# Optimization experiments

Measured on AMD Instinct MI355X. Metric: run time of the kernel, lower is better.

The kernel has to match this reference:

```python
import jax, jax.numpy as jnp
import numpy as np

N, M, D, K = 32768, 8192, 384, 9


def setup_inputs() -> dict:
    key = jax.random.key(0)
    k1, k2 = jax.random.split(key)
    return {
        "embedding": jax.random.normal(k1, (N, D), dtype=jnp.float32),
        "memory_bank": jax.random.normal(k2, (M, D), dtype=jnp.float32),
        "n_neighbors": K,
    }


def reference(embedding, memory_bank, n_neighbors):
    x_norm = jnp.sum(embedding * embedding, axis=-1, keepdims=True)      # [N, 1]
    y_norm = jnp.sum(memory_bank * memory_bank, axis=-1, keepdims=True)  # [M, 1]
    d2 = x_norm - 2.0 * jnp.matmul(embedding, memory_bank.T) + y_norm.T  # [N, M]
    dist = jnp.sqrt(jnp.maximum(d2, 0.0))
    # topk smallest along dim 1 (patch_scores, indices discarded)
    neg_top, _ = jax.lax.top_k(-dist, n_neighbors)
    patch_scores = -neg_top  # [N, K], ascending distances
    return patch_scores
```

## Files before the change

kernel.cpp:

```cpp
#include <hip/hip_runtime.h>
#include <hip/hip_bf16.h>

#define N_ROWS 32768
#define M_ROWS 8192
#define D_DIM  384
#define K_NB   9
#define BN     32
#define BM     128
#define NMQ    4
#define MQ     (M_ROWS / NMQ)
#define TILES  (MQ / BN)
#define KS     3

#define QSCALE (1.0f / 2048.0f)
#define YOFF   0.125f
#define QSTEPF (2048.0f / 65535.0f)
#define QOFFB  256.0f
#define M2S    (-2.0f / 2048.0f)
#define BIGF   3.0e38f

#define BUFSZ  12288
#define YS_OFF 24576

typedef __attribute__((ext_vector_type(4))) int      i32x4;
typedef __attribute__((ext_vector_type(8))) int      i32x8;
typedef __attribute__((ext_vector_type(4))) float    f32x4;
typedef __attribute__((ext_vector_type(4))) unsigned u32x4;

#define GLDS(SRC, DST)                                                       \
  __builtin_amdgcn_global_load_lds(                                          \
      (const __attribute__((address_space(1))) void*)(SRC),                  \
      (__attribute__((address_space(3))) void*)(DST), 16, 0, 0)

#define MF(AF, B, C)                                                         \
  __builtin_amdgcn_mfma_scale_f32_16x16x128_f8f6f4(                          \
      (AF), (B), (C), 0, 0, 0, 0x7F7F7F7F, 0, 0x7F7F7F7F)

__global__ __launch_bounds__(256) void FAPM_prep8(
    const float* __restrict__ emb, const float* __restrict__ mem,
    unsigned* __restrict__ A8, unsigned* __restrict__ B8,
    float* __restrict__ xn, float* __restrict__ yn) {
  const int lane = threadIdx.x & 63;
  const int row  = blockIdx.x * 4 + (threadIdx.x >> 6);
  const float* src;
  unsigned* dst;
  float* nptr;
  if (row < N_ROWS) {
    src = emb + (size_t)row * D_DIM; dst = A8 + (size_t)row * 96; nptr = xn + row;
  } else {
    int r = row - N_ROWS;
    src = mem + (size_t)r * D_DIM; dst = B8 + (size_t)r * 96; nptr = yn + r;
  }
  float s = 0.f;
  {
    int dw = lane;
    f32x4 v = *(const f32x4*)(src + dw * 4);
    s += v.x * v.x + v.y * v.y + v.z * v.z + v.w * v.w;
    int pk = __builtin_amdgcn_cvt_pk_fp8_f32(v.x, v.y, 0, false);
    pk = __builtin_amdgcn_cvt_pk_fp8_f32(v.z, v.w, pk, true);
    dst[dw] = (unsigned)pk;
  }
  if (lane < 32) {
    int dw = lane + 64;
    f32x4 v = *(const f32x4*)(src + dw * 4);
    s += v.x * v.x + v.y * v.y + v.z * v.z + v.w * v.w;
    int pk = __builtin_amdgcn_cvt_pk_fp8_f32(v.x, v.y, 0, false);
    pk = __builtin_amdgcn_cvt_pk_fp8_f32(v.z, v.w, pk, true);
    dst[dw] = (unsigned)pk;
  }
#pragma unroll
  for (int dd = 1; dd < 64; dd <<= 1) s += __shfl_xor(s, dd);
  if (lane == 0) *nptr = s;
}

__device__ __forceinline__ unsigned pkmin(unsigned a, unsigned b) {
  unsigned d;
  asm("v_pk_min_u16 %0, %1, %2" : "=v"(d) : "v"(a), "v"(b));
  return d;
}
__device__ __forceinline__ unsigned pkmax(unsigned a, unsigned b) {
  unsigned d;
  asm("v_pk_max_u16 %0, %1, %2" : "=v"(d) : "v"(a), "v"(b));
  return d;
}

__device__ __forceinline__ void merge16i(unsigned t[9], float* dst, int sub) {
  for (int s = 0; s < K_NB; ++s) {
    unsigned m  = t[0];
    int      ml = sub;
#pragma unroll
    for (int dd = 1; dd < 16; dd <<= 1) {
      unsigned ov = (unsigned)__shfl_xor((int)m, dd);
      int      ol = __shfl_xor(ml, dd);
      bool take = (ov < m) || (ov == m && ol < ml);
      m  = take ? ov : m;
      ml = take ? ol : ml;
    }
    if (sub == ml) {
#pragma unroll
      for (int j = 0; j < 8; ++j) t[j] = t[j + 1];
      t[8] = 0xFFFFu;
    }
    if (sub == 0) dst[s] = (float)m * QSTEPF - QOFFB;
  }
}

__global__ __launch_bounds__(256, 4) void FAPM_fused(
    const unsigned char* __restrict__ A8, const unsigned char* __restrict__ B8,
    const float* __restrict__ yn, float* __restrict__ part) {
  __shared__ __attribute__((aligned(128))) unsigned char LDS[28672];
  const int tid  = threadIdx.x;
  const int lane = tid & 63;
  const int w    = tid >> 6;
  const int sub  = lane & 15;
  const int grp  = lane >> 4;
  const int bx   = blockIdx.x;
  const int mq   = bx & (NMQ - 1);
  const int row0 = (bx >> 2) * BM;
  const int colbase = mq * MQ;

  {
    const float* yp = yn + colbase + tid * 8;
    f32x4 v0 = *(const f32x4*)yp;
    f32x4 v1 = *(const f32x4*)(yp + 4);
    float a0 = fmaf(v0.x, QSCALE, YOFF), a1 = fmaf(v0.y, QSCALE, YOFF);
    float a2 = fmaf(v0.z, QSCALE, YOFF), a3 = fmaf(v0.w, QSCALE, YOFF);
    float a4 = fmaf(v1.x, QSCALE, YOFF), a5 = fmaf(v1.y, QSCALE, YOFF);
    float a6 = fmaf(v1.z, QSCALE, YOFF), a7 = fmaf(v1.w, QSCALE, YOFF);
    unsigned q0, q1, q2, q3;
    asm("v_cvt_pknorm_u16_f32 %0, %1, %2" : "=v"(q0) : "v"(a0), "v"(a1));
    asm("v_cvt_pknorm_u16_f32 %0, %1, %2" : "=v"(q1) : "v"(a2), "v"(a3));
    asm("v_cvt_pknorm_u16_f32 %0, %1, %2" : "=v"(q2) : "v"(a4), "v"(a5));
    asm("v_cvt_pknorm_u16_f32 %0, %1, %2" : "=v"(q3) : "v"(a6), "v"(a7));
    *(u32x4*)(&LDS[YS_OFF + tid * 16]) = (u32x4){q0, q1, q2, q3};
  }

  i32x8 af[2][KS];

#pragma unroll
  for (int r = 0; r < 2; ++r) {
    const unsigned char* asrc =
        A8 + (size_t)(row0 + r * 64 + w * 16 + sub) * D_DIM + grp * 32;
#pragma unroll
    for (int ks = 0; ks < KS; ++ks)
#pragma unroll
      for (int h = 0; h < 2; ++h)
        GLDS(asrc + ks * 128 + h * 16, LDS + (w * 6 + ks * 2 + h) * 1024);
    asm volatile("s_waitcnt vmcnt(0)" ::: "memory");
    __syncthreads();
    if ((w >> 1) == r) {
#pragma unroll
      for (int rbl = 0; rbl < 2; ++rbl) {
        const int g = (w & 1) * 2 + rbl;
#pragma unroll
        for (int ks = 0; ks < KS; ++ks) {
          const unsigned char* p = LDS + (g * 6 + ks * 2) * 1024 + lane * 16;
          *(i32x4*)&af[rbl][ks] = *(const i32x4*)p;
          *((i32x4*)&af[rbl][ks] + 1) = *(const i32x4*)(p + 1024);
        }
      }
    }
    __syncthreads();
  }

  const unsigned char* bp0;
  const unsigned char* bp1;
  const unsigned char* bp2;
  int bd0, bd1, bd2;
  {
#pragma unroll
    for (int j = 0; j < 3; ++j) {
      int uu = w * 3 + j;
      int cb = uu / 6;
      int rem = uu - cb * 6;
      int ks = rem >> 1, h = rem & 1;
      const unsigned char* sp =
          B8 + (size_t)(colbase + cb * 16 + sub) * D_DIM + grp * 32 + ks * 128 + h * 16;
      int df = uu * 1024;
      if (j == 0) { bp0 = sp; bd0 = df; }
      else if (j == 1) { bp1 = sp; bd1 = df; }
      else { bp2 = sp; bd2 = df; }
    }
  }

  GLDS(bp0, LDS + bd0); GLDS(bp1, LDS + bd1); GLDS(bp2, LDS + bd2);
  GLDS(bp0 + BUFSZ, LDS + BUFSZ + bd0);
  GLDS(bp1 + BUFSZ, LDS + BUFSZ + bd1);
  GLDS(bp2 + BUFSZ, LDS + BUFSZ + bd2);
  bp0 += 2 * BUFSZ; bp1 += 2 * BUFSZ; bp2 += 2 * BUFSZ;

  unsigned tkp[4][9];
#pragma unroll
  for (int i = 0; i < 4; ++i)
#pragma unroll
    for (int j = 0; j < 9; ++j) tkp[i][j] = 0xFFFFFFFFu;

  for (int t = 0; t < TILES; ++t) {
    const int bufo = (t & 1) * BUFSZ;
    if (t + 1 < TILES) asm volatile("s_waitcnt vmcnt(3)" ::: "memory");
    else               asm volatile("s_waitcnt vmcnt(0)" ::: "memory");
    __builtin_amdgcn_s_barrier();

    const unsigned char* br = LDS + bufo + lane * 16;
#pragma unroll
    for (int cb = 0; cb < 2; ++cb) {
      unsigned yu = *(const unsigned short*)(
          &LDS[YS_OFF + ((t * BN + cb * 16 + sub) << 1)]);
      float ysv = (float)yu * (1.0f / 65535.0f);

      f32x4 acc0 = {0.f, 0.f, 0.f, 0.f}, acc1 = {0.f, 0.f, 0.f, 0.f};
      __builtin_amdgcn_s_setprio(1);
#pragma unroll
      for (int ks = 0; ks < KS; ++ks) {
        i32x8 b;
        const unsigned char* p = br + cb * 6144 + ks * 2048;
        *(i32x4*)&b = *(const i32x4*)p;
        *((i32x4*)&b + 1) = *(const i32x4*)(p + 1024);
        acc0 = MF(af[0][ks], b, acc0);
        acc1 = MF(af[1][ks], b, acc1);
      }
      __builtin_amdgcn_s_setprio(0);

#pragma unroll
      for (int i = 0; i < 4; ++i) {
        float d2a = fmaf(acc0[i], M2S, ysv);
        float d2b = fmaf(acc1[i], M2S, ysv);
        unsigned dp;
        asm("v_cvt_pknorm_u16_f32 %0, %1, %2" : "=v"(dp) : "v"(d2a), "v"(d2b));
#pragma unroll
        for (int j = 8; j >= 1; --j)
          tkp[i][j] = pkmin(tkp[i][j], pkmax(dp, tkp[i][j - 1]));
        tkp[i][0] = pkmin(tkp[i][0], dp);
      }
    }
    __builtin_amdgcn_s_barrier();

    if (t + 2 < TILES) {
      GLDS(bp0, LDS + bufo + bd0);
      GLDS(bp1, LDS + bufo + bd1);
      GLDS(bp2, LDS + bufo + bd2);
      bp0 += BUFSZ; bp1 += BUFSZ; bp2 += BUFSZ;
    }
  }

  float* pbase = part + (size_t)mq * N_ROWS * K_NB;
#pragma unroll
  for (int i = 0; i < 4; ++i) {
    unsigned ta[9], tb[9];
#pragma unroll
    for (int j = 0; j < 9; ++j) { ta[j] = tkp[i][j] & 0xFFFFu; tb[j] = tkp[i][j] >> 16; }
    int rowA = row0 + w * 32 + grp * 4 + i;
    merge16i(ta, pbase + (size_t)rowA * K_NB, sub);
    merge16i(tb, pbase + (size_t)(rowA + 16) * K_NB, sub);
  }
}

__global__ __launch_bounds__(256) void FAPM_merge4(
    const float* __restrict__ part, const float* __restrict__ xn,
    float* __restrict__ out) {
  const int r = blockIdx.x * 256 + threadIdx.x;
  const float xr = xn[r];
  float l[4][9];
#pragma unroll
  for (int q = 0; q < 4; ++q)
#pragma unroll
    for (int j = 0; j < 9; ++j)
      l[q][j] = part[(size_t)q * N_ROWS * K_NB + (size_t)r * K_NB + j];
#pragma unroll
  for (int s = 0; s < K_NB; ++s) {
    float m = fminf(fminf(l[0][0], l[1][0]), fminf(l[2][0], l[3][0]));
    out[(size_t)r * K_NB + s] = sqrtf(fmaxf(m + xr, 0.f));
    bool t0 = (l[0][0] == m);
    bool t1 = (l[1][0] == m) && !t0;
    bool t2 = (l[2][0] == m) && !t0 && !t1;
    bool t3 = !(t0 || t1 || t2);
#pragma unroll
    for (int j = 0; j < 8; ++j) {
      l[0][j] = t0 ? l[0][j + 1] : l[0][j];
      l[1][j] = t1 ? l[1][j + 1] : l[1][j];
      l[2][j] = t2 ? l[2][j + 1] : l[2][j];
      l[3][j] = t3 ? l[3][j + 1] : l[3][j];
    }
    l[0][8] = t0 ? BIGF : l[0][8];
    l[1][8] = t1 ? BIGF : l[1][8];
    l[2][8] = t2 ? BIGF : l[2][8];
    l[3][8] = t3 ? BIGF : l[3][8];
  }
}

extern "C" void kernel_launch(void* const* d_in, const int* in_sizes, int n_in,
                              void* d_out, int out_size, void* d_ws, size_t ws_size,
                              hipStream_t stream) {
  const float* emb = (const float*)d_in[0];
  const float* mem = (const float*)d_in[1];
  float* out = (float*)d_out;
  char* ws = (char*)d_ws;
  size_t offA = 0;
  size_t offB = offA + (size_t)N_ROWS * D_DIM;
  size_t offX = offB + (size_t)M_ROWS * D_DIM;
  size_t offY = offX + (size_t)N_ROWS * 4;
  size_t offP = offY + (size_t)M_ROWS * 4;
  unsigned char* A8 = (unsigned char*)(ws + offA);
  unsigned char* B8 = (unsigned char*)(ws + offB);
  float* xn = (float*)(ws + offX);
  float* yn = (float*)(ws + offY);
  float* part = (float*)(ws + offP);

  FAPM_prep8<<<(N_ROWS + M_ROWS) / 4, 256, 0, stream>>>(
      emb, mem, (unsigned*)A8, (unsigned*)B8, xn, yn);
  FAPM_fused<<<(N_ROWS / BM) * NMQ, 256, 0, stream>>>(A8, B8, yn, part);
  FAPM_merge4<<<N_ROWS / 256, 256, 0, stream>>>(part, xn, out);
}
```

Measured before the change: 183.0 us.

## Split memory bank into eight column slices and merge eight partial top-k lists

Doubles the number of M-dimension slices per row block, so the fused kernel launches twice as many blocks, each covering half as many column tiles. This is meant to improve occupancy and load balance across CUs. B staging is rewritten so waves pair up per 16-column block, and the y-norm LDS buffer is halved. The merge kernel now combines eight partial lists (two 4-way merges plus a 2-way merge), which doubles partial-result traffic and merge work.

```diff
diff --git a/kernel.cpp b/kernel.cpp
--- a/kernel.cpp
+++ b/kernel.cpp
@@ -7,7 +7,7 @@
 #define K_NB   9
 #define BN     32
 #define BM     128
-#define NMQ    4
+#define NMQ    8
 #define MQ     (M_ROWS / NMQ)
 #define TILES  (MQ / BN)
 #define KS     3
@@ -25,7 +25,7 @@
 typedef __attribute__((ext_vector_type(4))) int      i32x4;
 typedef __attribute__((ext_vector_type(8))) int      i32x8;
 typedef __attribute__((ext_vector_type(4))) float    f32x4;
-typedef __attribute__((ext_vector_type(4))) unsigned u32x4;
+typedef __attribute__((ext_vector_type(2))) unsigned u32x2;
 
 #define GLDS(SRC, DST)                                                       \
   __builtin_amdgcn_global_load_lds(                                          \
@@ -105,10 +105,21 @@
   }
 }
 
+#define STAGE_B(GB, DSTO)                                                    \
+  if ((w & 1) == 0) {                                                        \
+    GLDS((GB), LDS + (DSTO));                                                \
+    GLDS((GB) + 16, LDS + (DSTO) + 1024);                                    \
+    GLDS((GB) + 128, LDS + (DSTO) + 2048);                                   \
+  } else {                                                                   \
+    GLDS((GB) + 144, LDS + (DSTO));                                          \
+    GLDS((GB) + 256, LDS + (DSTO) + 1024);                                   \
+    GLDS((GB) + 272, LDS + (DSTO) + 2048);                                   \
+  }
+
 __global__ __launch_bounds__(256, 4) void FAPM_fused(
     const unsigned char* __restrict__ A8, const unsigned char* __restrict__ B8,
     const float* __restrict__ yn, float* __restrict__ part) {
-  __shared__ __attribute__((aligned(128))) unsigned char LDS[28672];
+  __shared__ __attribute__((aligned(128))) unsigned char LDS[26624];
   const int tid  = threadIdx.x;
   const int lane = tid & 63;
   const int w    = tid >> 6;
@@ -116,10 +127,10 @@
   const int grp  = lane >> 4;
   const int bx   = blockIdx.x;
   const int mq   = bx & (NMQ - 1);
-  const int row0 = (bx >> 2) * BM;
+  const int row0 = (bx >> 3) * BM;
   const int colbase = mq * MQ;
 
-  {
+  if (tid < 128) {
     const float* yp = yn + colbase + tid * 8;
     f32x4 v0 = *(const f32x4*)yp;
     f32x4 v1 = *(const f32x4*)(yp + 4);
@@ -132,7 +143,8 @@
     asm("v_cvt_pknorm_u16_f32 %0, %1, %2" : "=v"(q1) : "v"(a2), "v"(a3));
     asm("v_cvt_pknorm_u16_f32 %0, %1, %2" : "=v"(q2) : "v"(a4), "v"(a5));
     asm("v_cvt_pknorm_u16_f32 %0, %1, %2" : "=v"(q3) : "v"(a6), "v"(a7));
-    *(u32x4*)(&LDS[YS_OFF + tid * 16]) = (u32x4){q0, q1, q2, q3};
+    *(u32x2*)(&LDS[YS_OFF + tid * 16]) = (u32x2){q0, q1};
+    *(u32x2*)(&LDS[YS_OFF + tid * 16 + 8]) = (u32x2){q2, q3};
   }
 
   i32x8 af[2][KS];
@@ -163,31 +175,13 @@
     __syncthreads();
   }
 
-  const unsigned char* bp0;
-  const unsigned char* bp1;
-  const unsigned char* bp2;
-  int bd0, bd1, bd2;
-  {
-#pragma unroll
-    for (int j = 0; j < 3; ++j) {
-      int uu = w * 3 + j;
-      int cb = uu / 6;
-      int rem = uu - cb * 6;
-      int ks = rem >> 1, h = rem & 1;
-      const unsigned char* sp =
-          B8 + (size_t)(colbase + cb * 16 + sub) * D_DIM + grp * 32 + ks * 128 + h * 16;
-      int df = uu * 1024;
-      if (j == 0) { bp0 = sp; bd0 = df; }
-      else if (j == 1) { bp1 = sp; bd1 = df; }
-      else { bp2 = sp; bd2 = df; }
-    }
-  }
-
-  GLDS(bp0, LDS + bd0); GLDS(bp1, LDS + bd1); GLDS(bp2, LDS + bd2);
-  GLDS(bp0 + BUFSZ, LDS + BUFSZ + bd0);
-  GLDS(bp1 + BUFSZ, LDS + BUFSZ + bd1);
-  GLDS(bp2 + BUFSZ, LDS + BUFSZ + bd2);
-  bp0 += 2 * BUFSZ; bp1 += 2 * BUFSZ; bp2 += 2 * BUFSZ;
+  const unsigned char* bbase =
+      B8 + (size_t)(colbase + (w >> 1) * 16 + sub) * D_DIM + grp * 32;
+  const int bdst = w * 3 * 1024;
+
+  STAGE_B(bbase, bdst);
+  STAGE_B(bbase + BUFSZ, BUFSZ + bdst);
+  bbase += 2 * BUFSZ;
 
   unsigned tkp[4][9];
 #pragma unroll
@@ -236,10 +230,8 @@
     __builtin_amdgcn_s_barrier();
 
     if (t + 2 < TILES) {
-      GLDS(bp0, LDS + bufo + bd0);
-      GLDS(bp1, LDS + bufo + bd1);
-      GLDS(bp2, LDS + bufo + bd2);
-      bp0 += BUFSZ; bp1 += BUFSZ; bp2 += BUFSZ;
+      STAGE_B(bbase, bufo + bdst);
+      bbase += BUFSZ;
     }
   }
 
@@ -255,21 +247,11 @@
   }
 }
 
-__global__ __launch_bounds__(256) void FAPM_merge4(
-    const float* __restrict__ part, const float* __restrict__ xn,
-    float* __restrict__ out) {
-  const int r = blockIdx.x * 256 + threadIdx.x;
-  const float xr = xn[r];
-  float l[4][9];
-#pragma unroll
-  for (int q = 0; q < 4; ++q)
-#pragma unroll
-    for (int j = 0; j < 9; ++j)
-      l[q][j] = part[(size_t)q * N_ROWS * K_NB + (size_t)r * K_NB + j];
+__device__ __forceinline__ void merge4lists(float l[4][9], float o[9]) {
 #pragma unroll
   for (int s = 0; s < K_NB; ++s) {
     float m = fminf(fminf(l[0][0], l[1][0]), fminf(l[2][0], l[3][0]));
-    out[(size_t)r * K_NB + s] = sqrtf(fmaxf(m + xr, 0.f));
+    o[s] = m;
     bool t0 = (l[0][0] == m);
     bool t1 = (l[1][0] == m) && !t0;
     bool t2 = (l[2][0] == m) && !t0 && !t1;
@@ -285,6 +267,40 @@
     l[1][8] = t1 ? BIGF : l[1][8];
     l[2][8] = t2 ? BIGF : l[2][8];
     l[3][8] = t3 ? BIGF : l[3][8];
+  }
+}
+
+__global__ __launch_bounds__(256) void FAPM_merge8(
+    const float* __restrict__ part, const float* __restrict__ xn,
+    float* __restrict__ out) {
+  const int r = blockIdx.x * 256 + threadIdx.x;
+  const float xr = xn[r];
+  float l[4][9], a[9], b[9];
+#pragma unroll
+  for (int q = 0; q < 4; ++q)
+#pragma unroll
+    for (int j = 0; j < 9; ++j)
+      l[q][j] = part[(size_t)q * N_ROWS * K_NB + (size_t)r * K_NB + j];
+  merge4lists(l, a);
+#pragma unroll
+  for (int q = 0; q < 4; ++q)
+#pragma unroll
+    for (int j = 0; j < 9; ++j)
+      l[q][j] = part[(size_t)(q + 4) * N_ROWS * K_NB + (size_t)r * K_NB + j];
+  merge4lists(l, b);
+#pragma unroll
+  for (int s = 0; s < K_NB; ++s) {
+    bool ta = a[0] <= b[0];
+    float m = ta ? a[0] : b[0];
+    out[(size_t)r * K_NB + s] = sqrtf(fmaxf(m + xr, 0.f));
+#pragma unroll
+    for (int j = 0; j < 8; ++j) {
+      float an = a[j + 1], bn = b[j + 1];
+      a[j] = ta ? an : a[j];
+      b[j] = ta ? b[j] : bn;
+    }
+    a[8] = ta ? BIGF : a[8];
+    b[8] = ta ? b[8] : BIGF;
   }
 }
 
@@ -309,5 +325,5 @@
   FAPM_prep8<<<(N_ROWS + M_ROWS) / 4, 256, 0, stream>>>(
       emb, mem, (unsigned*)A8, (unsigned*)B8, xn, yn);
   FAPM_fused<<<(N_ROWS / BM) * NMQ, 256, 0, stream>>>(A8, B8, yn, part);
-  FAPM_merge4<<<N_ROWS / 256, 256, 0, stream>>>(part, xn, out);
-}
+  FAPM_merge8<<<N_ROWS / 256, 256, 0, stream>>>(part, xn, out);
+}
```

New measurement: 194.6 us. 1.06x slower.

## Give each wave private B staging buffers and drop block-wide barriers

Applied to the files above, without the earlier changes.

Each wave now streams its own copy of the B tile (16 columns per step) into a private double-buffered LDS region, so the per-tile s_barrier pairs go away and waves run independently. The next tile's loads are issued right after the current tile's LDS reads, before the MFMAs. The cost is four-fold redundant global-to-LDS traffic for B and a much larger LDS footprint, with launch bounds lowered from 4 to 3 blocks per CU. The loop also runs twice as many iterations, each doing half the work.

```diff
diff --git a/kernel.cpp b/kernel.cpp
--- a/kernel.cpp
+++ b/kernel.cpp
@@ -5,7 +5,7 @@
 #define M_ROWS 8192
 #define D_DIM  384
 #define K_NB   9
-#define BN     32
+#define BN     16
 #define BM     128
 #define NMQ    4
 #define MQ     (M_ROWS / NMQ)
@@ -19,8 +19,9 @@
 #define M2S    (-2.0f / 2048.0f)
 #define BIGF   3.0e38f
 
-#define BUFSZ  12288
-#define YS_OFF 24576
+#define BUFSZ  6144
+#define WBUF   12288
+#define YS_OFF 49152
 
 typedef __attribute__((ext_vector_type(4))) int      i32x4;
 typedef __attribute__((ext_vector_type(8))) int      i32x8;
@@ -105,10 +106,20 @@
   }
 }
 
-__global__ __launch_bounds__(256, 4) void FAPM_fused(
+#define STAGE_B(GB, DSTO)                                                    \
+  {                                                                          \
+    GLDS((GB), LDS + (DSTO));                                                \
+    GLDS((GB) + 16, LDS + (DSTO) + 1024);                                    \
+    GLDS((GB) + 128, LDS + (DSTO) + 2048);                                   \
+    GLDS((GB) + 144, LDS + (DSTO) + 3072);                                   \
+    GLDS((GB) + 256, LDS + (DSTO) + 4096);                                   \
+    GLDS((GB) + 272, LDS + (DSTO) + 5120);                                   \
+  }
+
+__global__ __launch_bounds__(256, 3) void FAPM_fused(
     const unsigned char* __restrict__ A8, const unsigned char* __restrict__ B8,
     const float* __restrict__ yn, float* __restrict__ part) {
-  __shared__ __attribute__((aligned(128))) unsigned char LDS[28672];
+  __shared__ __attribute__((aligned(128))) unsigned char LDS[53248];
   const int tid  = threadIdx.x;
   const int lane = tid & 63;
   const int w    = tid >> 6;
@@ -163,31 +174,12 @@
     __syncthreads();
   }
 
-  const unsigned char* bp0;
-  const unsigned char* bp1;
-  const unsigned char* bp2;
-  int bd0, bd1, bd2;
-  {
-#pragma unroll
-    for (int j = 0; j < 3; ++j) {
-      int uu = w * 3 + j;
-      int cb = uu / 6;
-      int rem = uu - cb * 6;
-      int ks = rem >> 1, h = rem & 1;
-      const unsigned char* sp =
-          B8 + (size_t)(colbase + cb * 16 + sub) * D_DIM + grp * 32 + ks * 128 + h * 16;
-      int df = uu * 1024;
-      if (j == 0) { bp0 = sp; bd0 = df; }
-      else if (j == 1) { bp1 = sp; bd1 = df; }
-      else { bp2 = sp; bd2 = df; }
-    }
-  }
-
-  GLDS(bp0, LDS + bd0); GLDS(bp1, LDS + bd1); GLDS(bp2, LDS + bd2);
-  GLDS(bp0 + BUFSZ, LDS + BUFSZ + bd0);
-  GLDS(bp1 + BUFSZ, LDS + BUFSZ + bd1);
-  GLDS(bp2 + BUFSZ, LDS + BUFSZ + bd2);
-  bp0 += 2 * BUFSZ; bp1 += 2 * BUFSZ; bp2 += 2 * BUFSZ;
+  const unsigned char* gb =
+      B8 + (size_t)(colbase + sub) * D_DIM + grp * 32;
+  const int wbase = w * WBUF;
+  STAGE_B(gb, wbase);
+  STAGE_B(gb + 6144, wbase + BUFSZ);
+  const unsigned char* gbs = gb + 2 * 6144;
 
   unsigned tkp[4][9];
 #pragma unroll
@@ -196,50 +188,46 @@
     for (int j = 0; j < 9; ++j) tkp[i][j] = 0xFFFFFFFFu;
 
   for (int t = 0; t < TILES; ++t) {
-    const int bufo = (t & 1) * BUFSZ;
-    if (t + 1 < TILES) asm volatile("s_waitcnt vmcnt(3)" ::: "memory");
+    const int bufo = wbase + (t & 1) * BUFSZ;
+    if (t + 1 < TILES) asm volatile("s_waitcnt vmcnt(6)" ::: "memory");
     else               asm volatile("s_waitcnt vmcnt(0)" ::: "memory");
-    __builtin_amdgcn_s_barrier();
 
     const unsigned char* br = LDS + bufo + lane * 16;
-#pragma unroll
-    for (int cb = 0; cb < 2; ++cb) {
-      unsigned yu = *(const unsigned short*)(
-          &LDS[YS_OFF + ((t * BN + cb * 16 + sub) << 1)]);
-      float ysv = (float)yu * (1.0f / 65535.0f);
-
-      f32x4 acc0 = {0.f, 0.f, 0.f, 0.f}, acc1 = {0.f, 0.f, 0.f, 0.f};
-      __builtin_amdgcn_s_setprio(1);
-#pragma unroll
-      for (int ks = 0; ks < KS; ++ks) {
-        i32x8 b;
-        const unsigned char* p = br + cb * 6144 + ks * 2048;
-        *(i32x4*)&b = *(const i32x4*)p;
-        *((i32x4*)&b + 1) = *(const i32x4*)(p + 1024);
-        acc0 = MF(af[0][ks], b, acc0);
-        acc1 = MF(af[1][ks], b, acc1);
-      }
-      __builtin_amdgcn_s_setprio(0);
-
-#pragma unroll
-      for (int i = 0; i < 4; ++i) {
-        float d2a = fmaf(acc0[i], M2S, ysv);
-        float d2b = fmaf(acc1[i], M2S, ysv);
-        unsigned dp;
-        asm("v_cvt_pknorm_u16_f32 %0, %1, %2" : "=v"(dp) : "v"(d2a), "v"(d2b));
-#pragma unroll
-        for (int j = 8; j >= 1; --j)
-          tkp[i][j] = pkmin(tkp[i][j], pkmax(dp, tkp[i][j - 1]));
-        tkp[i][0] = pkmin(tkp[i][0], dp);
-      }
-    }
-    __builtin_amdgcn_s_barrier();
-
+    i32x8 b0, b1, b2;
+    *(i32x4*)&b0 = *(const i32x4*)br;
+    *((i32x4*)&b0 + 1) = *(const i32x4*)(br + 1024);
+    *(i32x4*)&b1 = *(const i32x4*)(br + 2048);
+    *((i32x4*)&b1 + 1) = *(const i32x4*)(br + 3072);
+    *(i32x4*)&b2 = *(const i32x4*)(br + 4096);
+    *((i32x4*)&b2 + 1) = *(const i32x4*)(br + 5120);
+    unsigned yu = *(const unsigned short*)(
+        &LDS[YS_OFF + ((t * BN + sub) << 1)]);
+    float ysv = (float)yu * (1.0f / 65535.0f);
+
+    asm volatile("s_waitcnt lgkmcnt(0)" ::: "memory");
     if (t + 2 < TILES) {
-      GLDS(bp0, LDS + bufo + bd0);
-      GLDS(bp1, LDS + bufo + bd1);
-      GLDS(bp2, LDS + bufo + bd2);
-      bp0 += BUFSZ; bp1 += BUFSZ; bp2 += BUFSZ;
+      STAGE_B(gbs, bufo);
+      gbs += 6144;
+    }
+
+    f32x4 acc0 = {0.f, 0.f, 0.f, 0.f}, acc1 = {0.f, 0.f, 0.f, 0.f};
+    acc0 = MF(af[0][0], b0, acc0);
+    acc1 = MF(af[1][0], b0, acc1);
+    acc0 = MF(af[0][1], b1, acc0);
+    acc1 = MF(af[1][1], b1, acc1);
+    acc0 = MF(af[0][2], b2, acc0);
+    acc1 = MF(af[1][2], b2, acc1);
+
+#pragma unroll
+    for (int i = 0; i < 4; ++i) {
+      float d2a = fmaf(acc0[i], M2S, ysv);
+      float d2b = fmaf(acc1[i], M2S, ysv);
+      unsigned dp;
+      asm("v_cvt_pknorm_u16_f32 %0, %1, %2" : "=v"(dp) : "v"(d2a), "v"(d2b));
+#pragma unroll
+      for (int j = 8; j >= 1; --j)
+        tkp[i][j] = pkmin(tkp[i][j], pkmax(dp, tkp[i][j - 1]));
+      tkp[i][0] = pkmin(tkp[i][0], dp);
     }
   }
 
```

After: 382.7 us. +109.1%, slower.
